# Kernel tuning notes

Measured on AMD Instinct MI355X. Metric: run time of the kernel, lower is better.

Reference implementation:

```python
import jax, jax.numpy as jnp
import numpy as np

B, S, SK = 4, 1024, 1024
Q_IN, KV_IN = 1024, 1024
G, DQ, DV = 16, 64, 64
OUT = Q_IN
EPS = 1e-5


def setup_inputs() -> dict:
    key = jax.random.key(0)
    ks = jax.random.split(key, 12)
    s_q = 1.0 / np.sqrt(Q_IN)
    s_kv = 1.0 / np.sqrt(KV_IN)
    s_p = 1.0 / np.sqrt(G * DV)
    return {
        "Q": jax.random.normal(ks[0], (B, S, Q_IN), jnp.float32),
        "KV": jax.random.normal(ks[1], (B, SK, KV_IN), jnp.float32),
        "Wq": jax.random.normal(ks[2], (G * DQ, Q_IN), jnp.float32) * s_q,
        "bq": jax.random.normal(ks[3], (G * DQ,), jnp.float32) * s_q,
        "Wk": jax.random.normal(ks[4], (G * DQ, KV_IN), jnp.float32) * s_kv,
        "bk": jax.random.normal(ks[5], (G * DQ,), jnp.float32) * s_kv,
        "Wv": jax.random.normal(ks[6], (G * DV, KV_IN), jnp.float32) * s_kv,
        "bv": jax.random.normal(ks[7], (G * DV,), jnp.float32) * s_kv,
        "Wp": jax.random.normal(ks[8], (OUT, G * DV), jnp.float32) * s_p,
        "bp": jax.random.normal(ks[9], (OUT,), jnp.float32) * s_p,
        "gamma": jnp.ones((OUT,), jnp.float32),
        "beta": jnp.zeros((OUT,), jnp.float32),
    }


def reference(Q, KV, Wq, bq, Wk, bk, Wv, bv, Wp, bp, gamma, beta):
    b, s, _ = Q.shape
    sk = KV.shape[1]
    inv_sqrt_dim = DQ ** (-0.5)

    # projections
    q = Q @ Wq.T + bq            # [b, s, G*DQ]
    k = KV @ Wk.T + bk           # [b, sk, G*DQ]
    v = KV @ Wv.T + bv           # [b, sk, G*DV]

    # q/k: group is the SLOW axis; v: group is the FAST axis (faithful to source)
    q = q.reshape(b, s, G, DQ)               # [b, s, g, d]
    k = k.reshape(b, sk, G, DQ)              # [b, sk, g, d]
    v = v.reshape(b, sk, DV, G)              # [b, sk, d, g]

    logits = jnp.einsum('bsgd,btgd->bgst', q, k) * inv_sqrt_dim  # [b, g, s, sk]
    scores = jax.nn.softmax(logits, axis=-1)
    attn = jnp.einsum('bgst,btdg->bgsd', scores, v)              # [b, g, s, dv]

    # flatten as (dv, g): feature index = d*G + g  (faithful to source permute)
    attn = attn.transpose(0, 2, 3, 1).reshape(b, s, DV * G)
    out = attn @ Wp.T + bp + Q

    # LayerNorm
    mu = out.mean(axis=-1, keepdims=True)
    var = out.var(axis=-1, keepdims=True)
    out = (out - mu) * jax.lax.rsqrt(var + EPS) * gamma + beta

    return out, scores.reshape(b * G, s, sk)
```

## Files before the change

### kernel.cpp

```cpp
#include <hip/hip_runtime.h>

typedef __attribute__((ext_vector_type(8))) short short8;
typedef __attribute__((ext_vector_type(4))) short s16x4;
typedef __attribute__((ext_vector_type(4))) float f32x4;
typedef __attribute__((ext_vector_type(2))) unsigned u32x2;

static __device__ __forceinline__ short f2bf(float x) {
  union { float f; unsigned u; } v; v.f = x;
  unsigned r = (v.u + 0x7fffu + ((v.u >> 16) & 1u)) >> 16;
  return (short)r;
}
static __device__ __forceinline__ unsigned cvtpk(float lo, float hi) {
  unsigned r;
  asm("v_cvt_pk_bf16_f32 %0, %1, %2" : "=v"(r) : "v"(lo), "v"(hi));
  return r;
}

static __device__ __forceinline__ void gld16(const short* g, short* l) {
  __builtin_amdgcn_global_load_lds(
      (const __attribute__((address_space(1))) unsigned*)g,
      (__attribute__((address_space(3))) unsigned*)l, 16, 0, 0);
}

static __device__ __forceinline__ void conv8(const float* __restrict__ src,
                                             short* __restrict__ dst, int i,
                                             float scale) {
  const f32x4* s = (const f32x4*)(src + (long)i * 8);
  f32x4 a = s[0], b = s[1];
  short8 o;
  o[0] = f2bf(a[0] * scale); o[1] = f2bf(a[1] * scale);
  o[2] = f2bf(a[2] * scale); o[3] = f2bf(a[3] * scale);
  o[4] = f2bf(b[0] * scale); o[5] = f2bf(b[1] * scale);
  o[6] = f2bf(b[2] * scale); o[7] = f2bf(b[3] * scale);
  *(short8*)(dst + (long)i * 8) = o;
}

__global__ __launch_bounds__(256) void prep(
    const float* __restrict__ Q, const float* __restrict__ KV,
    const float* __restrict__ Wq, const float* __restrict__ Wk,
    const float* __restrict__ Wv, const float* __restrict__ Wp,
    const float* __restrict__ bq,
    short* __restrict__ Qb, short* __restrict__ KVb,
    short* __restrict__ Wqb, short* __restrict__ Wkb,
    short* __restrict__ Wvb, short* __restrict__ Wpb,
    float* __restrict__ bqs) {
  const int blk = blockIdx.x, tid = threadIdx.x;
  if (blk < 2048) {
    conv8(Q, Qb, blk * 256 + tid, 1.f);
  } else if (blk < 4096) {
    conv8(KV, KVb, (blk - 2048) * 256 + tid, 1.f);
  } else if (blk < 4608) {
    conv8(Wq, Wqb, (blk - 4096) * 256 + tid, 0.125f);
  } else if (blk < 5120) {
    conv8(Wk, Wkb, (blk - 4608) * 256 + tid, 1.f);
  } else if (blk < 5632) {
    conv8(Wv, Wvb, (blk - 5120) * 256 + tid, 1.f);
  } else if (blk < 6656) {
    __shared__ float row[1024];
    const long o = blk - 5632;
    *(f32x4*)&row[tid * 4] = *(const f32x4*)(Wp + o * 1024 + tid * 4);
    __syncthreads();
    const int f0 = tid * 4;
    s16x4 t;
#pragma unroll
    for (int j = 0; j < 4; ++j) {
      int f = f0 + j;
      t[j] = f2bf(row[((f & 63) << 4) + (f >> 6)]);
    }
    *(s16x4*)(Wpb + o * 1024 + f0) = t;
  } else {
    int i = (blk - 6656) * 256 + tid;
    bqs[i] = bq[i] * 0.125f;
  }
}

template <typename OutT>
static __device__ __forceinline__ void gemm_core(
    const short* __restrict__ A, const short* __restrict__ B,
    OutT* __restrict__ C, const float* __restrict__ bias,
    const float* __restrict__ resid, int bm, int bn, int omode,
    short* Sm) {
  const int tid = threadIdx.x, lane = tid & 63, wave = tid >> 6;
  const int fr = lane & 15, khi = lane >> 4;
  const int wr = wave >> 1, wc = wave & 1;

  f32x4 acc[4][4];
#pragma unroll
  for (int m = 0; m < 4; ++m)
#pragma unroll
    for (int n = 0; n < 4; ++n) acc[m][n] = (f32x4){0.f, 0.f, 0.f, 0.f};

  auto stage = [&](int buf, int k0) {
    short* Asb = Sm + buf * 16384;
    short* Bsb = Asb + 8192;
#pragma unroll
    for (int it = 0; it < 4; ++it) {
      int l = it * 256 + tid;
      int r = l >> 3, c = (l & 7) ^ (r & 7);
      gld16(A + (long)(bm + r) * 1024 + k0 + c * 8, &Asb[l * 8]);
      gld16(B + (long)(bn + r) * 1024 + k0 + c * 8, &Bsb[l * 8]);
    }
  };

  stage(0, 0);
  __syncthreads();
  int cur = 0;
  for (int k0 = 0; k0 < 1024; k0 += 64) {
    if (k0 < 960) stage(cur ^ 1, k0 + 64);
    const short* Asb = Sm + cur * 16384;
    const short* Bsb = Asb + 8192;
#pragma unroll
    for (int ks = 0; ks < 64; ks += 32) {
      const int cc = (ks >> 3) + khi;
      short8 af[4], bf[4];
#pragma unroll
      for (int m = 0; m < 4; ++m) {
        const int ar = wr * 64 + m * 16 + fr;
        af[m] = *(const short8*)&Asb[ar * 64 + ((cc ^ (ar & 7)) * 8)];
      }
#pragma unroll
      for (int n = 0; n < 4; ++n) {
        const int br = wc * 64 + n * 16 + fr;
        bf[n] = *(const short8*)&Bsb[br * 64 + ((cc ^ (br & 7)) * 8)];
      }
#pragma unroll
      for (int m = 0; m < 4; ++m)
#pragma unroll
        for (int n = 0; n < 4; ++n)
          acc[m][n] = __builtin_amdgcn_mfma_f32_16x16x32_bf16(af[m], bf[n],
                                                              acc[m][n], 0, 0, 0);
    }
    __syncthreads();
    cur ^= 1;
  }

  const int col0 = fr, row0 = khi * 4;
  if constexpr (sizeof(OutT) == 2) {
#pragma unroll
    for (int m = 0; m < 4; ++m) {
#pragma unroll
      for (int n = 0; n < 4; ++n) {
        const int dgl = wc * 64 + n * 16 + col0;
        const float bi = bias[bn + dgl];
#pragma unroll
        for (int i = 0; i < 4; ++i) {
          const int tl = wr * 64 + m * 16 + row0 + i;
          const int a = (omode == 1) ? (dgl * 136 + tl) : (tl * 136 + dgl);
          Sm[a] = f2bf(acc[m][n][i] + bi);
        }
      }
    }
    __syncthreads();
    short* Cs = (short*)C;
#pragma unroll
    for (int it = 0; it < 8; ++it) {
      const int ch = it * 256 + tid;
      const int r = ch >> 4, cchunk = ch & 15;
      short8 v8 = *(const short8*)&Sm[r * 136 + cchunk * 8];
      long addr;
      if (omode == 0)
        addr = (long)(bm + r) * 1024 + bn + cchunk * 8;
      else
        addr = ((long)(bm >> 10) << 20) + ((long)(bn + r) << 10) + (bm & 1023) +
               cchunk * 8;
      *(short8*)(Cs + addr) = v8;
    }
  } else {
#pragma unroll
    for (int m = 0; m < 4; ++m) {
#pragma unroll
      for (int n = 0; n < 4; ++n) {
        const int gcol = bn + wc * 64 + n * 16 + col0;
        const float bi = bias[gcol];
#pragma unroll
        for (int i = 0; i < 4; ++i) {
          const int grow = bm + wr * 64 + m * 16 + row0 + i;
          float v = acc[m][n][i] + bi;
          if (resid) v += resid[(long)grow * 1024 + gcol];
          C[(long)grow * 1024 + gcol] = v;
        }
      }
    }
  }
}

__global__ __launch_bounds__(256, 2) void proj_all(
    const short* __restrict__ Qb, const short* __restrict__ KVb,
    const short* __restrict__ Wqb, const short* __restrict__ Wkb,
    const short* __restrict__ Wvb,
    const float* __restrict__ bqs, const float* __restrict__ bk,
    const float* __restrict__ bv,
    short* __restrict__ qb, short* __restrict__ kb, short* __restrict__ vt) {
  __shared__ short Sm[32768];
  int bid = blockIdx.x;
  int swz = (bid & 7) * 96 + (bid >> 3);
  const int seg = swz >> 8, local = swz & 255;
  const int bm = (local >> 3) * 128, bn = (local & 7) * 128;
  if (seg == 0)
    gemm_core<short>(Qb, Wqb, qb, bqs, nullptr, bm, bn, 0, Sm);
  else if (seg == 1)
    gemm_core<short>(KVb, Wkb, kb, bk, nullptr, bm, bn, 0, Sm);
  else
    gemm_core<short>(KVb, Wvb, vt, bv, nullptr, bm, bn, 1, Sm);
}

__global__ __launch_bounds__(256, 2) void out_gemm(
    const short* __restrict__ at, const short* __restrict__ Wpb,
    const float* __restrict__ bp, const float* __restrict__ Q,
    float* __restrict__ pre) {
  __shared__ short Sm[32768];
  int bid = blockIdx.x;
  int swz = (bid & 7) * 32 + (bid >> 3);
  const int bm = (swz >> 3) * 128, bn = (swz & 7) * 128;
  gemm_core<float>(at, Wpb, pre, bp, Q, bm, bn, 0, Sm);
}

__global__ __launch_bounds__(256, 3) void fused_attn(
    const short* __restrict__ qb,
    const short* __restrict__ kb,
    const short* __restrict__ vt,
    float* __restrict__ scores,
    short* __restrict__ at) {
  constexpr int LP = 72;
  __shared__ short Ks[2][64 * 64];
  __shared__ short Vs[2][64 * 64];
  __shared__ short Ps[128 * LP];

  int bid = blockIdx.x;
  bid = (bid & 7) * 64 + (bid >> 3);
  const int z = bid >> 3, b = z >> 4, g = z & 15;
  const int q0 = (bid & 7) * 128;

  const int tid = threadIdx.x, lane = tid & 63, w = tid >> 6;
  const int fr = lane & 15, khi = lane >> 4;
  const long bqk = (long)b << 20;
  const int qr = q0 + w * 32;

  short8 aq[4];
#pragma unroll
  for (int sub = 0; sub < 2; ++sub) {
    const short* qrow = qb + bqk + (long)(qr + sub * 16 + fr) * 1024 + g * 64 + khi * 8;
    aq[sub * 2] = *(const short8*)qrow;
    aq[sub * 2 + 1] = *(const short8*)(qrow + 32);
  }
  const short* kgp = kb + bqk + g * 64;
  const short* vgp = vt + bqk;

  auto stageK = [&](int buf, int t0) {
#pragma unroll
    for (int it = 0; it < 2; ++it) {
      int l = it * 256 + tid;
      int r = l >> 3, c = (l & 7) ^ ((l >> 5) & 7);
      gld16(kgp + (long)(t0 + r) * 1024 + c * 8, &Ks[buf][l * 8]);
    }
  };
  auto stageV = [&](int buf, int t0) {
#pragma unroll
    for (int it = 0; it < 2; ++it) {
      int l = it * 256 + tid;
      int r = l >> 3, c = (l & 7) ^ (r & 7);
      gld16(vgp + ((long)(r * 16 + g) << 10) + t0 + c * 8, &Vs[buf][l * 8]);
    }
  };

  const int xk = fr & 7;

  float s4[2][4] = {{0.f, 0.f, 0.f, 0.f}, {0.f, 0.f, 0.f, 0.f}};
  stageK(0, 0);
  __syncthreads();
  int cur = 0;
  for (int t0 = 0; t0 < 1024; t0 += 64) {
    if (t0 < 960) stageK(cur ^ 1, t0 + 64);
    f32x4 sacc[2][4];
#pragma unroll
    for (int sub = 0; sub < 2; ++sub)
#pragma unroll
      for (int nf = 0; nf < 4; ++nf) sacc[sub][nf] = (f32x4){0.f, 0.f, 0.f, 0.f};
#pragma unroll
    for (int nf = 0; nf < 4; ++nf) {
      const int r2 = fr * 4 + nf;
      short8 b0 = *(const short8*)&Ks[cur][r2 * 64 + ((khi ^ xk) * 8)];
      short8 b1 = *(const short8*)&Ks[cur][r2 * 64 + (((khi + 4) ^ xk) * 8)];
#pragma unroll
      for (int sub = 0; sub < 2; ++sub) {
        sacc[sub][nf] =
            __builtin_amdgcn_mfma_f32_16x16x32_bf16(aq[sub * 2], b0, sacc[sub][nf], 0, 0, 0);
        sacc[sub][nf] =
            __builtin_amdgcn_mfma_f32_16x16x32_bf16(aq[sub * 2 + 1], b1, sacc[sub][nf], 0, 0, 0);
      }
    }
#pragma unroll
    for (int sub = 0; sub < 2; ++sub)
#pragma unroll
      for (int nf = 0; nf < 4; ++nf)
#pragma unroll
        for (int i = 0; i < 4; ++i) s4[sub][i] += __expf(sacc[sub][nf][i]);
    __syncthreads();
    cur ^= 1;
  }
  float inv4[2][4];
#pragma unroll
  for (int sub = 0; sub < 2; ++sub)
#pragma unroll
    for (int i = 0; i < 4; ++i) {
      float s = s4[sub][i];
      s += __shfl_xor(s, 1);
      s += __shfl_xor(s, 2);
      s += __shfl_xor(s, 4);
      s += __shfl_xor(s, 8);
      inv4[sub][i] = 1.f / s;
    }

  f32x4 pacc[2][4];
#pragma unroll
  for (int sub = 0; sub < 2; ++sub)
#pragma unroll
    for (int nv = 0; nv < 4; ++nv) pacc[sub][nv] = (f32x4){0.f, 0.f, 0.f, 0.f};

  stageK(0, 0);
  stageV(0, 0);
  __syncthreads();
  cur = 0;
  for (int t0 = 0; t0 < 1024; t0 += 64) {
    if (t0 < 960) {
      stageK(cur ^ 1, t0 + 64);
      stageV(cur ^ 1, t0 + 64);
    }
    f32x4 sacc[2][4];
#pragma unroll
    for (int sub = 0; sub < 2; ++sub)
#pragma unroll
      for (int nf = 0; nf < 4; ++nf) sacc[sub][nf] = (f32x4){0.f, 0.f, 0.f, 0.f};
#pragma unroll
    for (int nf = 0; nf < 4; ++nf) {
      const int r2 = fr * 4 + nf;
      short8 b0 = *(const short8*)&Ks[cur][r2 * 64 + ((khi ^ xk) * 8)];
      short8 b1 = *(const short8*)&Ks[cur][r2 * 64 + (((khi + 4) ^ xk) * 8)];
#pragma unroll
      for (int sub = 0; sub < 2; ++sub) {
        sacc[sub][nf] =
            __builtin_amdgcn_mfma_f32_16x16x32_bf16(aq[sub * 2], b0, sacc[sub][nf], 0, 0, 0);
        sacc[sub][nf] =
            __builtin_amdgcn_mfma_f32_16x16x32_bf16(aq[sub * 2 + 1], b1, sacc[sub][nf], 0, 0, 0);
      }
    }
#pragma unroll
    for (int sub = 0; sub < 2; ++sub) {
#pragma unroll
      for (int i = 0; i < 4; ++i) {
        f32x4 o;
#pragma unroll
        for (int nf = 0; nf < 4; ++nf)
          o[nf] = __expf(sacc[sub][nf][i]) * inv4[sub][i];
        const int row = sub * 16 + khi * 4 + i;
        __builtin_nontemporal_store(
            o, (f32x4*)&scores[((long)z << 20) + ((long)(qr + row) << 10) + t0 + fr * 4]);
        u32x2 pp;
        pp[0] = cvtpk(o[0], o[1]);
        pp[1] = cvtpk(o[2], o[3]);
        *(u32x2*)&Ps[(w * 32 + row) * LP + fr * 4] = pp;
      }
    }

#pragma unroll
    for (int ks = 0; ks < 64; ks += 32) {
      const int cc = (ks >> 3) + khi;
      short8 ap[2];
#pragma unroll
      for (int sub = 0; sub < 2; ++sub)
        ap[sub] = *(const short8*)&Ps[(w * 32 + sub * 16 + fr) * LP + ks + khi * 8];
#pragma unroll
      for (int nv = 0; nv < 4; ++nv) {
        const int dr = nv * 16 + fr;
        short8 bvv = *(const short8*)&Vs[cur][dr * 64 + ((cc ^ (dr & 7)) * 8)];
#pragma unroll
        for (int sub = 0; sub < 2; ++sub)
          pacc[sub][nv] =
              __builtin_amdgcn_mfma_f32_16x16x32_bf16(ap[sub], bvv, pacc[sub][nv], 0, 0, 0);
      }
    }
    __syncthreads();
    cur ^= 1;
  }

#pragma unroll
  for (int sub = 0; sub < 2; ++sub)
#pragma unroll
    for (int nv = 0; nv < 4; ++nv)
#pragma unroll
      for (int i = 0; i < 4; ++i)
        Ps[(w * 32 + sub * 16 + khi * 4 + i) * LP + nv * 16 + fr] =
            f2bf(pacc[sub][nv][i]);
  const long atbase = bqk + ((long)qr << 10) + g * 64;
#pragma unroll
  for (int it = 0; it < 4; ++it) {
    const int ch = it * 64 + lane;
    const int row = ch >> 3, fc = ch & 7;
    s16x4 lo = *(const s16x4*)&Ps[(w * 32 + row) * LP + fc * 8];
    s16x4 hi = *(const s16x4*)&Ps[(w * 32 + row) * LP + fc * 8 + 4];
    short8 v8;
    v8[0] = lo[0]; v8[1] = lo[1]; v8[2] = lo[2]; v8[3] = lo[3];
    v8[4] = hi[0]; v8[5] = hi[1]; v8[6] = hi[2]; v8[7] = hi[3];
    *(short8*)(at + atbase + ((long)row << 10) + fc * 8) = v8;
  }
}

__global__ __launch_bounds__(256) void layernorm_rows(const float* __restrict__ X,
                                                      const float* __restrict__ gamma,
                                                      const float* __restrict__ beta,
                                                      float* __restrict__ O) {
  const int row = blockIdx.x * 4 + (threadIdx.x >> 6);
  const int lane = threadIdx.x & 63;
  const float* x = X + (long)row * 1024 + lane * 4;
  f32x4 v[4];
  float s = 0.f, sq = 0.f;
#pragma unroll
  for (int j = 0; j < 4; ++j) {
    v[j] = *(const f32x4*)(x + j * 256);
#pragma unroll
    for (int e = 0; e < 4; ++e) {
      s += v[j][e];
      sq += v[j][e] * v[j][e];
    }
  }
#pragma unroll
  for (int off = 32; off; off >>= 1) {
    s += __shfl_xor(s, off);
    sq += __shfl_xor(sq, off);
  }
  const float mu = s * (1.f / 1024.f);
  const float var = sq * (1.f / 1024.f) - mu * mu;
  const float rstd = rsqrtf(var + 1e-5f);
  float* o = O + (long)row * 1024 + lane * 4;
#pragma unroll
  for (int j = 0; j < 4; ++j) {
    f32x4 g = *(const f32x4*)(gamma + lane * 4 + j * 256);
    f32x4 be = *(const f32x4*)(beta + lane * 4 + j * 256);
    f32x4 r;
#pragma unroll
    for (int e = 0; e < 4; ++e) r[e] = (v[j][e] - mu) * rstd * g[e] + be[e];
    *(f32x4*)(o + j * 256) = r;
  }
}

extern "C" void kernel_launch(void* const* d_in, const int* in_sizes, int n_in,
                              void* d_out, int out_size, void* d_ws, size_t ws_size,
                              hipStream_t stream) {
  const float* Q = (const float*)d_in[0];
  const float* KV = (const float*)d_in[1];
  const float* Wq = (const float*)d_in[2];
  const float* bq = (const float*)d_in[3];
  const float* Wk = (const float*)d_in[4];
  const float* bk = (const float*)d_in[5];
  const float* Wv = (const float*)d_in[6];
  const float* bv = (const float*)d_in[7];
  const float* Wp = (const float*)d_in[8];
  const float* bp = (const float*)d_in[9];
  const float* gamma = (const float*)d_in[10];
  const float* beta = (const float*)d_in[11];

  float* out = (float*)d_out;
  float* scores = out + (long)4 * 1024 * 1024;

  char* ws = (char*)d_ws;
  short* Wqb = (short*)(ws);
  short* Wkb = (short*)(ws + (2L << 20));
  short* Wvb = (short*)(ws + (4L << 20));
  short* Wpb = (short*)(ws + (6L << 20));
  short* qb  = (short*)(ws + (8L << 20));
  short* kb  = (short*)(ws + (16L << 20));
  short* vt  = (short*)(ws + (24L << 20));
  short* at  = (short*)(ws + (32L << 20));
  float* pre = (float*)(ws + (40L << 20));
  short* Qb  = (short*)(ws + (40L << 20));
  short* KVb = (short*)(ws + (48L << 20));
  float* bqs = (float*)(ws + (56L << 20));
  (void)ws_size; (void)in_sizes; (void)n_in; (void)out_size;

  prep<<<6660, 256, 0, stream>>>(Q, KV, Wq, Wk, Wv, Wp, bq,
                                 Qb, KVb, Wqb, Wkb, Wvb, Wpb, bqs);

  proj_all<<<768, 256, 0, stream>>>(Qb, KVb, Wqb, Wkb, Wvb, bqs, bk, bv,
                                    qb, kb, vt);

  fused_attn<<<512, 256, 0, stream>>>(qb, kb, vt, scores, at);

  out_gemm<<<256, 256, 0, stream>>>(at, Wpb, bp, Q, pre);

  layernorm_rows<<<1024, 256, 0, stream>>>(pre, gamma, beta, out);
}
```

Baseline: 164.9 us.

## Split softmax row-sum pass into a separate higher-occupancy kernel

Moves the first attention pass, which computes the exp row sums of QK^T, out of the fused attention kernel into its own kernel. The new kernel uses 64-row query tiles, 1024 blocks and launch bounds of 4, and writes the inverse sums to a workspace buffer. The emit kernel then reads those inverses and runs only the second pass, which writes the scores and computes P·V. This is meant to give more parallelism and occupancy for the sum pass, at the cost of an extra launch, a small global round trip, and recomputing QK per 64-row tile with less reuse of K.

```diff
diff --git a/kernel.cpp b/kernel.cpp
--- a/kernel.cpp
+++ b/kernel.cpp
@@ -215,10 +215,76 @@
   gemm_core<float>(at, Wpb, pre, bp, Q, bm, bn, 0, Sm);
 }
 
-__global__ __launch_bounds__(256, 3) void fused_attn(
+__global__ __launch_bounds__(256, 4) void attn_sums(
+    const short* __restrict__ qb, const short* __restrict__ kb,
+    float* __restrict__ sinv) {
+  __shared__ short Ks[2][64 * 64];
+  int bid = blockIdx.x;
+  bid = (bid & 7) * 128 + (bid >> 3);
+  const int z = bid >> 4, b = z >> 4, g = z & 15;
+  const int q0 = (bid & 15) * 64;
+
+  const int tid = threadIdx.x, lane = tid & 63, w = tid >> 6;
+  const int fr = lane & 15, khi = lane >> 4;
+  const long bqk = (long)b << 20;
+  const int qr = q0 + w * 16;
+
+  const short* qrow = qb + bqk + (long)(qr + fr) * 1024 + g * 64 + khi * 8;
+  const short8 aq0 = *(const short8*)qrow;
+  const short8 aq1 = *(const short8*)(qrow + 32);
+  const short* kgp = kb + bqk + g * 64;
+
+  auto stageK = [&](int buf, int t0) {
+#pragma unroll
+    for (int it = 0; it < 2; ++it) {
+      int l = it * 256 + tid;
+      int r = l >> 3, c = (l & 7) ^ (r & 7);
+      gld16(kgp + (long)(t0 + r) * 1024 + c * 8, &Ks[buf][l * 8]);
+    }
+  };
+
+  float s4[4] = {0.f, 0.f, 0.f, 0.f};
+  stageK(0, 0);
+  __syncthreads();
+  int cur = 0;
+  const int xk = fr & 7;
+  for (int t0 = 0; t0 < 1024; t0 += 64) {
+    if (t0 < 960) stageK(cur ^ 1, t0 + 64);
+#pragma unroll
+    for (int nf = 0; nf < 4; ++nf) {
+      const int r2 = nf * 16 + fr;
+      short8 b0 = *(const short8*)&Ks[cur][r2 * 64 + ((khi ^ xk) * 8)];
+      short8 b1 = *(const short8*)&Ks[cur][r2 * 64 + (((khi + 4) ^ xk) * 8)];
+      f32x4 sacc = (f32x4){0.f, 0.f, 0.f, 0.f};
+      sacc = __builtin_amdgcn_mfma_f32_16x16x32_bf16(aq0, b0, sacc, 0, 0, 0);
+      sacc = __builtin_amdgcn_mfma_f32_16x16x32_bf16(aq1, b1, sacc, 0, 0, 0);
+#pragma unroll
+      for (int i = 0; i < 4; ++i) s4[i] += __expf(sacc[i]);
+    }
+    __syncthreads();
+    cur ^= 1;
+  }
+#pragma unroll
+  for (int i = 0; i < 4; ++i) {
+    float s = s4[i];
+    s += __shfl_xor(s, 1);
+    s += __shfl_xor(s, 2);
+    s += __shfl_xor(s, 4);
+    s += __shfl_xor(s, 8);
+    s4[i] = s;
+  }
+  if (fr == 0) {
+#pragma unroll
+    for (int i = 0; i < 4; ++i)
+      sinv[(long)z * 1024 + qr + khi * 4 + i] = 1.f / s4[i];
+  }
+}
+
+__global__ __launch_bounds__(256, 3) void attn_emit(
     const short* __restrict__ qb,
     const short* __restrict__ kb,
     const short* __restrict__ vt,
+    const float* __restrict__ sinv,
     float* __restrict__ scores,
     short* __restrict__ at) {
   constexpr int LP = 72;
@@ -243,6 +309,13 @@
     aq[sub * 2] = *(const short8*)qrow;
     aq[sub * 2 + 1] = *(const short8*)(qrow + 32);
   }
+  float inv4[2][4];
+#pragma unroll
+  for (int sub = 0; sub < 2; ++sub)
+#pragma unroll
+    for (int i = 0; i < 4; ++i)
+      inv4[sub][i] = sinv[(long)z * 1024 + qr + sub * 16 + khi * 4 + i];
+
   const short* kgp = kb + bqk + g * 64;
   const short* vgp = vt + bqk;
 
@@ -265,52 +338,6 @@
 
   const int xk = fr & 7;
 
-  float s4[2][4] = {{0.f, 0.f, 0.f, 0.f}, {0.f, 0.f, 0.f, 0.f}};
-  stageK(0, 0);
-  __syncthreads();
-  int cur = 0;
-  for (int t0 = 0; t0 < 1024; t0 += 64) {
-    if (t0 < 960) stageK(cur ^ 1, t0 + 64);
-    f32x4 sacc[2][4];
-#pragma unroll
-    for (int sub = 0; sub < 2; ++sub)
-#pragma unroll
-      for (int nf = 0; nf < 4; ++nf) sacc[sub][nf] = (f32x4){0.f, 0.f, 0.f, 0.f};
-#pragma unroll
-    for (int nf = 0; nf < 4; ++nf) {
-      const int r2 = fr * 4 + nf;
-      short8 b0 = *(const short8*)&Ks[cur][r2 * 64 + ((khi ^ xk) * 8)];
-      short8 b1 = *(const short8*)&Ks[cur][r2 * 64 + (((khi + 4) ^ xk) * 8)];
-#pragma unroll
-      for (int sub = 0; sub < 2; ++sub) {
-        sacc[sub][nf] =
-            __builtin_amdgcn_mfma_f32_16x16x32_bf16(aq[sub * 2], b0, sacc[sub][nf], 0, 0, 0);
-        sacc[sub][nf] =
-            __builtin_amdgcn_mfma_f32_16x16x32_bf16(aq[sub * 2 + 1], b1, sacc[sub][nf], 0, 0, 0);
-      }
-    }
-#pragma unroll
-    for (int sub = 0; sub < 2; ++sub)
-#pragma unroll
-      for (int nf = 0; nf < 4; ++nf)
-#pragma unroll
-        for (int i = 0; i < 4; ++i) s4[sub][i] += __expf(sacc[sub][nf][i]);
-    __syncthreads();
-    cur ^= 1;
-  }
-  float inv4[2][4];
-#pragma unroll
-  for (int sub = 0; sub < 2; ++sub)
-#pragma unroll
-    for (int i = 0; i < 4; ++i) {
-      float s = s4[sub][i];
-      s += __shfl_xor(s, 1);
-      s += __shfl_xor(s, 2);
-      s += __shfl_xor(s, 4);
-      s += __shfl_xor(s, 8);
-      inv4[sub][i] = 1.f / s;
-    }
-
   f32x4 pacc[2][4];
 #pragma unroll
   for (int sub = 0; sub < 2; ++sub)
@@ -320,7 +347,7 @@
   stageK(0, 0);
   stageV(0, 0);
   __syncthreads();
-  cur = 0;
+  int cur = 0;
   for (int t0 = 0; t0 < 1024; t0 += 64) {
     if (t0 < 960) {
       stageK(cur ^ 1, t0 + 64);
@@ -475,6 +502,7 @@
   short* Qb  = (short*)(ws + (40L << 20));
   short* KVb = (short*)(ws + (48L << 20));
   float* bqs = (float*)(ws + (56L << 20));
+  float* sinv = (float*)(ws + (56L << 20) + 65536);
   (void)ws_size; (void)in_sizes; (void)n_in; (void)out_size;
 
   prep<<<6660, 256, 0, stream>>>(Q, KV, Wq, Wk, Wv, Wp, bq,
@@ -483,7 +511,9 @@
   proj_all<<<768, 256, 0, stream>>>(Qb, KVb, Wqb, Wkb, Wvb, bqs, bk, bv,
                                     qb, kb, vt);
 
-  fused_attn<<<512, 256, 0, stream>>>(qb, kb, vt, scores, at);
+  attn_sums<<<1024, 256, 0, stream>>>(qb, kb, sinv);
+
+  attn_emit<<<512, 256, 0, stream>>>(qb, kb, vt, sinv, scores, at);
 
   out_gemm<<<256, 256, 0, stream>>>(at, Wpb, bp, Q, pre);
 
```

After: 167.1 us. About the same (+1.4%).

## Fuse fp32-to-bf16 activation conversion into projection GEMM and single-buffer attention

Applied to the files above, without the earlier changes.

The separate prep pass that converted Q and KV to bf16 is removed. The projection GEMM now loads fp32 activations directly, converts them in registers and writes bf16 into LDS, which saves a full write-and-reread of the activations through global memory. The catch is that A-tile staging becomes synchronous register loads instead of async global-to-LDS loads. Separately, fused_attn drops its K/V double buffering in favour of single buffers with a barrier per tile, and raises its occupancy hint from 3 to 4 blocks. This trades load/compute overlap for more resident waves.

```diff
diff --git a/kernel.cpp b/kernel.cpp
--- a/kernel.cpp
+++ b/kernel.cpp
@@ -36,28 +36,22 @@
 }
 
 __global__ __launch_bounds__(256) void prep(
-    const float* __restrict__ Q, const float* __restrict__ KV,
     const float* __restrict__ Wq, const float* __restrict__ Wk,
     const float* __restrict__ Wv, const float* __restrict__ Wp,
     const float* __restrict__ bq,
-    short* __restrict__ Qb, short* __restrict__ KVb,
     short* __restrict__ Wqb, short* __restrict__ Wkb,
     short* __restrict__ Wvb, short* __restrict__ Wpb,
     float* __restrict__ bqs) {
   const int blk = blockIdx.x, tid = threadIdx.x;
-  if (blk < 2048) {
-    conv8(Q, Qb, blk * 256 + tid, 1.f);
-  } else if (blk < 4096) {
-    conv8(KV, KVb, (blk - 2048) * 256 + tid, 1.f);
-  } else if (blk < 4608) {
-    conv8(Wq, Wqb, (blk - 4096) * 256 + tid, 0.125f);
-  } else if (blk < 5120) {
-    conv8(Wk, Wkb, (blk - 4608) * 256 + tid, 1.f);
-  } else if (blk < 5632) {
-    conv8(Wv, Wvb, (blk - 5120) * 256 + tid, 1.f);
-  } else if (blk < 6656) {
+  if (blk < 512) {
+    conv8(Wq, Wqb, blk * 256 + tid, 0.125f);
+  } else if (blk < 1024) {
+    conv8(Wk, Wkb, (blk - 512) * 256 + tid, 1.f);
+  } else if (blk < 1536) {
+    conv8(Wv, Wvb, (blk - 1024) * 256 + tid, 1.f);
+  } else if (blk < 2560) {
     __shared__ float row[1024];
-    const long o = blk - 5632;
+    const long o = blk - 1536;
     *(f32x4*)&row[tid * 4] = *(const f32x4*)(Wp + o * 1024 + tid * 4);
     __syncthreads();
     const int f0 = tid * 4;
@@ -69,14 +63,14 @@
     }
     *(s16x4*)(Wpb + o * 1024 + f0) = t;
   } else {
-    int i = (blk - 6656) * 256 + tid;
+    int i = (blk - 2560) * 256 + tid;
     bqs[i] = bq[i] * 0.125f;
   }
 }
 
-template <typename OutT>
+template <bool AF32, typename OutT>
 static __device__ __forceinline__ void gemm_core(
-    const short* __restrict__ A, const short* __restrict__ B,
+    const void* __restrict__ Ap, const short* __restrict__ B,
     OutT* __restrict__ C, const float* __restrict__ bias,
     const float* __restrict__ resid, int bm, int bn, int omode,
     short* Sm) {
@@ -84,6 +78,9 @@
   const int fr = lane & 15, khi = lane >> 4;
   const int wr = wave >> 1, wc = wave & 1;
 
+  const short* A16 = AF32 ? nullptr : (const short*)Ap;
+  const float* A32 = AF32 ? (const float*)Ap : nullptr;
+
   f32x4 acc[4][4];
 #pragma unroll
   for (int m = 0; m < 4; ++m)
@@ -97,7 +94,17 @@
     for (int it = 0; it < 4; ++it) {
       int l = it * 256 + tid;
       int r = l >> 3, c = (l & 7) ^ (r & 7);
-      gld16(A + (long)(bm + r) * 1024 + k0 + c * 8, &Asb[l * 8]);
+      if (!AF32) {
+        gld16(A16 + (long)(bm + r) * 1024 + k0 + c * 8, &Asb[l * 8]);
+      } else {
+        const float* p = A32 + (long)(bm + r) * 1024 + k0 + c * 8;
+        f32x4 x = *(const f32x4*)p, y = *(const f32x4*)(p + 4);
+        u32x2 lo, hi;
+        lo[0] = cvtpk(x[0], x[1]); lo[1] = cvtpk(x[2], x[3]);
+        hi[0] = cvtpk(y[0], y[1]); hi[1] = cvtpk(y[2], y[3]);
+        *(u32x2*)&Asb[l * 8] = lo;
+        *(u32x2*)&Asb[l * 8 + 4] = hi;
+      }
       gld16(B + (long)(bn + r) * 1024 + k0 + c * 8, &Bsb[l * 8]);
     }
   };
@@ -185,7 +192,7 @@
 }
 
 __global__ __launch_bounds__(256, 2) void proj_all(
-    const short* __restrict__ Qb, const short* __restrict__ KVb,
+    const float* __restrict__ Q, const float* __restrict__ KV,
     const short* __restrict__ Wqb, const short* __restrict__ Wkb,
     const short* __restrict__ Wvb,
     const float* __restrict__ bqs, const float* __restrict__ bk,
@@ -197,11 +204,11 @@
   const int seg = swz >> 8, local = swz & 255;
   const int bm = (local >> 3) * 128, bn = (local & 7) * 128;
   if (seg == 0)
-    gemm_core<short>(Qb, Wqb, qb, bqs, nullptr, bm, bn, 0, Sm);
+    gemm_core<true, short>(Q, Wqb, qb, bqs, nullptr, bm, bn, 0, Sm);
   else if (seg == 1)
-    gemm_core<short>(KVb, Wkb, kb, bk, nullptr, bm, bn, 0, Sm);
+    gemm_core<true, short>(KV, Wkb, kb, bk, nullptr, bm, bn, 0, Sm);
   else
-    gemm_core<short>(KVb, Wvb, vt, bv, nullptr, bm, bn, 1, Sm);
+    gemm_core<true, short>(KV, Wvb, vt, bv, nullptr, bm, bn, 1, Sm);
 }
 
 __global__ __launch_bounds__(256, 2) void out_gemm(
@@ -212,18 +219,18 @@
   int bid = blockIdx.x;
   int swz = (bid & 7) * 32 + (bid >> 3);
   const int bm = (swz >> 3) * 128, bn = (swz & 7) * 128;
-  gemm_core<float>(at, Wpb, pre, bp, Q, bm, bn, 0, Sm);
-}
-
-__global__ __launch_bounds__(256, 3) void fused_attn(
+  gemm_core<false, float>(at, Wpb, pre, bp, Q, bm, bn, 0, Sm);
+}
+
+__global__ __launch_bounds__(256, 4) void fused_attn(
     const short* __restrict__ qb,
     const short* __restrict__ kb,
     const short* __restrict__ vt,
     float* __restrict__ scores,
     short* __restrict__ at) {
   constexpr int LP = 72;
-  __shared__ short Ks[2][64 * 64];
-  __shared__ short Vs[2][64 * 64];
+  __shared__ short Ks[64 * 64];
+  __shared__ short Vs[64 * 64];
   __shared__ short Ps[128 * LP];
 
   int bid = blockIdx.x;
@@ -246,31 +253,29 @@
   const short* kgp = kb + bqk + g * 64;
   const short* vgp = vt + bqk;
 
-  auto stageK = [&](int buf, int t0) {
+  auto stageK = [&](int t0) {
 #pragma unroll
     for (int it = 0; it < 2; ++it) {
       int l = it * 256 + tid;
       int r = l >> 3, c = (l & 7) ^ ((l >> 5) & 7);
-      gld16(kgp + (long)(t0 + r) * 1024 + c * 8, &Ks[buf][l * 8]);
+      gld16(kgp + (long)(t0 + r) * 1024 + c * 8, &Ks[l * 8]);
     }
   };
-  auto stageV = [&](int buf, int t0) {
+  auto stageV = [&](int t0) {
 #pragma unroll
     for (int it = 0; it < 2; ++it) {
       int l = it * 256 + tid;
       int r = l >> 3, c = (l & 7) ^ (r & 7);
-      gld16(vgp + ((long)(r * 16 + g) << 10) + t0 + c * 8, &Vs[buf][l * 8]);
+      gld16(vgp + ((long)(r * 16 + g) << 10) + t0 + c * 8, &Vs[l * 8]);
     }
   };
 
   const int xk = fr & 7;
 
   float s4[2][4] = {{0.f, 0.f, 0.f, 0.f}, {0.f, 0.f, 0.f, 0.f}};
-  stageK(0, 0);
-  __syncthreads();
-  int cur = 0;
   for (int t0 = 0; t0 < 1024; t0 += 64) {
-    if (t0 < 960) stageK(cur ^ 1, t0 + 64);
+    stageK(t0);
+    __syncthreads();
     f32x4 sacc[2][4];
 #pragma unroll
     for (int sub = 0; sub < 2; ++sub)
@@ -279,8 +284,8 @@
 #pragma unroll
     for (int nf = 0; nf < 4; ++nf) {
       const int r2 = fr * 4 + nf;
-      short8 b0 = *(const short8*)&Ks[cur][r2 * 64 + ((khi ^ xk) * 8)];
-      short8 b1 = *(const short8*)&Ks[cur][r2 * 64 + (((khi + 4) ^ xk) * 8)];
+      short8 b0 = *(const short8*)&Ks[r2 * 64 + ((khi ^ xk) * 8)];
+      short8 b1 = *(const short8*)&Ks[r2 * 64 + (((khi + 4) ^ xk) * 8)];
 #pragma unroll
       for (int sub = 0; sub < 2; ++sub) {
         sacc[sub][nf] =
@@ -296,7 +301,6 @@
 #pragma unroll
         for (int i = 0; i < 4; ++i) s4[sub][i] += __expf(sacc[sub][nf][i]);
     __syncthreads();
-    cur ^= 1;
   }
   float inv4[2][4];
 #pragma unroll
@@ -317,15 +321,10 @@
 #pragma unroll
     for (int nv = 0; nv < 4; ++nv) pacc[sub][nv] = (f32x4){0.f, 0.f, 0.f, 0.f};
 
-  stageK(0, 0);
-  stageV(0, 0);
-  __syncthreads();
-  cur = 0;
   for (int t0 = 0; t0 < 1024; t0 += 64) {
-    if (t0 < 960) {
-      stageK(cur ^ 1, t0 + 64);
-      stageV(cur ^ 1, t0 + 64);
-    }
+    stageK(t0);
+    stageV(t0);
+    __syncthreads();
     f32x4 sacc[2][4];
 #pragma unroll
     for (int sub = 0; sub < 2; ++sub)
@@ -334,8 +333,8 @@
 #pragma unroll
     for (int nf = 0; nf < 4; ++nf) {
       const int r2 = fr * 4 + nf;
-      short8 b0 = *(const short8*)&Ks[cur][r2 * 64 + ((khi ^ xk) * 8)];
-      short8 b1 = *(const short8*)&Ks[cur][r2 * 64 + (((khi + 4) ^ xk) * 8)];
+      short8 b0 = *(const short8*)&Ks[r2 * 64 + ((khi ^ xk) * 8)];
+      short8 b1 = *(const short8*)&Ks[r2 * 64 + (((khi + 4) ^ xk) * 8)];
 #pragma unroll
       for (int sub = 0; sub < 2; ++sub) {
         sacc[sub][nf] =
@@ -372,7 +371,7 @@
 #pragma unroll
       for (int nv = 0; nv < 4; ++nv) {
         const int dr = nv * 16 + fr;
-        short8 bvv = *(const short8*)&Vs[cur][dr * 64 + ((cc ^ (dr & 7)) * 8)];
+        short8 bvv = *(const short8*)&Vs[dr * 64 + ((cc ^ (dr & 7)) * 8)];
 #pragma unroll
         for (int sub = 0; sub < 2; ++sub)
           pacc[sub][nv] =
@@ -380,7 +379,6 @@
       }
     }
     __syncthreads();
-    cur ^= 1;
   }
 
 #pragma unroll
@@ -472,15 +470,12 @@
   short* vt  = (short*)(ws + (24L << 20));
   short* at  = (short*)(ws + (32L << 20));
   float* pre = (float*)(ws + (40L << 20));
-  short* Qb  = (short*)(ws + (40L << 20));
-  short* KVb = (short*)(ws + (48L << 20));
   float* bqs = (float*)(ws + (56L << 20));
   (void)ws_size; (void)in_sizes; (void)n_in; (void)out_size;
 
-  prep<<<6660, 256, 0, stream>>>(Q, KV, Wq, Wk, Wv, Wp, bq,
-                                 Qb, KVb, Wqb, Wkb, Wvb, Wpb, bqs);
-
-  proj_all<<<768, 256, 0, stream>>>(Qb, KVb, Wqb, Wkb, Wvb, bqs, bk, bv,
+  prep<<<2564, 256, 0, stream>>>(Wq, Wk, Wv, Wp, bq, Wqb, Wkb, Wvb, Wpb, bqs);
+
+  proj_all<<<768, 256, 0, stream>>>(Q, KV, Wqb, Wkb, Wvb, bqs, bk, bv,
                                     qb, kb, vt);
 
   fused_attn<<<512, 256, 0, stream>>>(qb, kb, vt, scores, at);
```

Result: slower. 186.5 us (+13.1%).

## Use 8 waves of 16 query rows each in fused attention

Applied to the files above, without the earlier changes.

The fused attention kernel now runs 512 threads per block, and each of the 8 waves handles 16 query rows instead of 32. Each thread issues one K/V staging load per tile instead of two. Per-wave register use drops, which allows more resident waves to hide the exp and scores-store latency. The cost is that each wave reuses each K/V LDS fragment for half as many MFMAs, and block-wide barriers now synchronise more waves.

```diff
diff --git a/kernel.cpp b/kernel.cpp
--- a/kernel.cpp
+++ b/kernel.cpp
@@ -215,7 +215,7 @@
   gemm_core<float>(at, Wpb, pre, bp, Q, bm, bn, 0, Sm);
 }
 
-__global__ __launch_bounds__(256, 3) void fused_attn(
+__global__ __launch_bounds__(512, 4) void fused_attn(
     const short* __restrict__ qb,
     const short* __restrict__ kb,
     const short* __restrict__ vt,
@@ -234,88 +234,63 @@
   const int tid = threadIdx.x, lane = tid & 63, w = tid >> 6;
   const int fr = lane & 15, khi = lane >> 4;
   const long bqk = (long)b << 20;
-  const int qr = q0 + w * 32;
-
-  short8 aq[4];
-#pragma unroll
-  for (int sub = 0; sub < 2; ++sub) {
-    const short* qrow = qb + bqk + (long)(qr + sub * 16 + fr) * 1024 + g * 64 + khi * 8;
-    aq[sub * 2] = *(const short8*)qrow;
-    aq[sub * 2 + 1] = *(const short8*)(qrow + 32);
-  }
+  const int qr = q0 + w * 16;
+
+  const short* qrow = qb + bqk + (long)(qr + fr) * 1024 + g * 64 + khi * 8;
+  const short8 aq0 = *(const short8*)qrow;
+  const short8 aq1 = *(const short8*)(qrow + 32);
   const short* kgp = kb + bqk + g * 64;
   const short* vgp = vt + bqk;
 
   auto stageK = [&](int buf, int t0) {
-#pragma unroll
-    for (int it = 0; it < 2; ++it) {
-      int l = it * 256 + tid;
-      int r = l >> 3, c = (l & 7) ^ ((l >> 5) & 7);
-      gld16(kgp + (long)(t0 + r) * 1024 + c * 8, &Ks[buf][l * 8]);
-    }
+    int r = tid >> 3, c = (tid & 7) ^ ((tid >> 5) & 7);
+    gld16(kgp + (long)(t0 + r) * 1024 + c * 8, &Ks[buf][tid * 8]);
   };
   auto stageV = [&](int buf, int t0) {
-#pragma unroll
-    for (int it = 0; it < 2; ++it) {
-      int l = it * 256 + tid;
-      int r = l >> 3, c = (l & 7) ^ (r & 7);
-      gld16(vgp + ((long)(r * 16 + g) << 10) + t0 + c * 8, &Vs[buf][l * 8]);
-    }
+    int r = tid >> 3, c = (tid & 7) ^ (r & 7);
+    gld16(vgp + ((long)(r * 16 + g) << 10) + t0 + c * 8, &Vs[buf][tid * 8]);
   };
 
   const int xk = fr & 7;
 
-  float s4[2][4] = {{0.f, 0.f, 0.f, 0.f}, {0.f, 0.f, 0.f, 0.f}};
+  float s4[4] = {0.f, 0.f, 0.f, 0.f};
   stageK(0, 0);
   __syncthreads();
   int cur = 0;
   for (int t0 = 0; t0 < 1024; t0 += 64) {
     if (t0 < 960) stageK(cur ^ 1, t0 + 64);
-    f32x4 sacc[2][4];
-#pragma unroll
-    for (int sub = 0; sub < 2; ++sub)
-#pragma unroll
-      for (int nf = 0; nf < 4; ++nf) sacc[sub][nf] = (f32x4){0.f, 0.f, 0.f, 0.f};
+    f32x4 sacc[4];
+#pragma unroll
+    for (int nf = 0; nf < 4; ++nf) sacc[nf] = (f32x4){0.f, 0.f, 0.f, 0.f};
 #pragma unroll
     for (int nf = 0; nf < 4; ++nf) {
       const int r2 = fr * 4 + nf;
       short8 b0 = *(const short8*)&Ks[cur][r2 * 64 + ((khi ^ xk) * 8)];
       short8 b1 = *(const short8*)&Ks[cur][r2 * 64 + (((khi + 4) ^ xk) * 8)];
-#pragma unroll
-      for (int sub = 0; sub < 2; ++sub) {
-        sacc[sub][nf] =
-            __builtin_amdgcn_mfma_f32_16x16x32_bf16(aq[sub * 2], b0, sacc[sub][nf], 0, 0, 0);
-        sacc[sub][nf] =
-            __builtin_amdgcn_mfma_f32_16x16x32_bf16(aq[sub * 2 + 1], b1, sacc[sub][nf], 0, 0, 0);
-      }
-    }
-#pragma unroll
-    for (int sub = 0; sub < 2; ++sub)
-#pragma unroll
-      for (int nf = 0; nf < 4; ++nf)
-#pragma unroll
-        for (int i = 0; i < 4; ++i) s4[sub][i] += __expf(sacc[sub][nf][i]);
+      sacc[nf] = __builtin_amdgcn_mfma_f32_16x16x32_bf16(aq0, b0, sacc[nf], 0, 0, 0);
+      sacc[nf] = __builtin_amdgcn_mfma_f32_16x16x32_bf16(aq1, b1, sacc[nf], 0, 0, 0);
+    }
+#pragma unroll
+    for (int nf = 0; nf < 4; ++nf)
+#pragma unroll
+      for (int i = 0; i < 4; ++i) s4[i] += __expf(sacc[nf][i]);
     __syncthreads();
     cur ^= 1;
   }
-  float inv4[2][4];
-#pragma unroll
-  for (int sub = 0; sub < 2; ++sub)
-#pragma unroll
-    for (int i = 0; i < 4; ++i) {
-      float s = s4[sub][i];
-      s += __shfl_xor(s, 1);
-      s += __shfl_xor(s, 2);
-      s += __shfl_xor(s, 4);
-      s += __shfl_xor(s, 8);
-      inv4[sub][i] = 1.f / s;
-    }
-
-  f32x4 pacc[2][4];
-#pragma unroll
-  for (int sub = 0; sub < 2; ++sub)
-#pragma unroll
-    for (int nv = 0; nv < 4; ++nv) pacc[sub][nv] = (f32x4){0.f, 0.f, 0.f, 0.f};
+  float inv4[4];
+#pragma unroll
+  for (int i = 0; i < 4; ++i) {
+    float s = s4[i];
+    s += __shfl_xor(s, 1);
+    s += __shfl_xor(s, 2);
+    s += __shfl_xor(s, 4);
+    s += __shfl_xor(s, 8);
+    inv4[i] = 1.f / s;
+  }
+
+  f32x4 pacc[4];
+#pragma unroll
+  for (int nv = 0; nv < 4; ++nv) pacc[nv] = (f32x4){0.f, 0.f, 0.f, 0.f};
 
   stageK(0, 0);
   stageV(0, 0);
@@ -326,57 +301,41 @@
       stageK(cur ^ 1, t0 + 64);
       stageV(cur ^ 1, t0 + 64);
     }
-    f32x4 sacc[2][4];
-#pragma unroll
-    for (int sub = 0; sub < 2; ++sub)
-#pragma unroll
-      for (int nf = 0; nf < 4; ++nf) sacc[sub][nf] = (f32x4){0.f, 0.f, 0.f, 0.f};
+    f32x4 sacc[4];
+#pragma unroll
+    for (int nf = 0; nf < 4; ++nf) sacc[nf] = (f32x4){0.f, 0.f, 0.f, 0.f};
 #pragma unroll
     for (int nf = 0; nf < 4; ++nf) {
       const int r2 = fr * 4 + nf;
       short8 b0 = *(const short8*)&Ks[cur][r2 * 64 + ((khi ^ xk) * 8)];
       short8 b1 = *(const short8*)&Ks[cur][r2 * 64 + (((khi + 4) ^ xk) * 8)];
-#pragma unroll
-      for (int sub = 0; sub < 2; ++sub) {
-        sacc[sub][nf] =
-            __builtin_amdgcn_mfma_f32_16x16x32_bf16(aq[sub * 2], b0, sacc[sub][nf], 0, 0, 0);
-        sacc[sub][nf] =
-            __builtin_amdgcn_mfma_f32_16x16x32_bf16(aq[sub * 2 + 1], b1, sacc[sub][nf], 0, 0, 0);
-      }
-    }
-#pragma unroll
-    for (int sub = 0; sub < 2; ++sub) {
-#pragma unroll
-      for (int i = 0; i < 4; ++i) {
-        f32x4 o;
-#pragma unroll
-        for (int nf = 0; nf < 4; ++nf)
-          o[nf] = __expf(sacc[sub][nf][i]) * inv4[sub][i];
-        const int row = sub * 16 + khi * 4 + i;
-        __builtin_nontemporal_store(
-            o, (f32x4*)&scores[((long)z << 20) + ((long)(qr + row) << 10) + t0 + fr * 4]);
-        u32x2 pp;
-        pp[0] = cvtpk(o[0], o[1]);
-        pp[1] = cvtpk(o[2], o[3]);
-        *(u32x2*)&Ps[(w * 32 + row) * LP + fr * 4] = pp;
-      }
+      sacc[nf] = __builtin_amdgcn_mfma_f32_16x16x32_bf16(aq0, b0, sacc[nf], 0, 0, 0);
+      sacc[nf] = __builtin_amdgcn_mfma_f32_16x16x32_bf16(aq1, b1, sacc[nf], 0, 0, 0);
+    }
+#pragma unroll
+    for (int i = 0; i < 4; ++i) {
+      f32x4 o;
+#pragma unroll
+      for (int nf = 0; nf < 4; ++nf)
+        o[nf] = __expf(sacc[nf][i]) * inv4[i];
+      const int row = khi * 4 + i;
+      __builtin_nontemporal_store(
+          o, (f32x4*)&scores[((long)z << 20) + ((long)(qr + row) << 10) + t0 + fr * 4]);
+      u32x2 pp;
+      pp[0] = cvtpk(o[0], o[1]);
+      pp[1] = cvtpk(o[2], o[3]);
+      *(u32x2*)&Ps[(w * 16 + row) * LP + fr * 4] = pp;
     }
 
 #pragma unroll
     for (int ks = 0; ks < 64; ks += 32) {
       const int cc = (ks >> 3) + khi;
-      short8 ap[2];
-#pragma unroll
-      for (int sub = 0; sub < 2; ++sub)
-        ap[sub] = *(const short8*)&Ps[(w * 32 + sub * 16 + fr) * LP + ks + khi * 8];
+      short8 ap = *(const short8*)&Ps[(w * 16 + fr) * LP + ks + khi * 8];
 #pragma unroll
       for (int nv = 0; nv < 4; ++nv) {
         const int dr = nv * 16 + fr;
         short8 bvv = *(const short8*)&Vs[cur][dr * 64 + ((cc ^ (dr & 7)) * 8)];
-#pragma unroll
-        for (int sub = 0; sub < 2; ++sub)
-          pacc[sub][nv] =
-              __builtin_amdgcn_mfma_f32_16x16x32_bf16(ap[sub], bvv, pacc[sub][nv], 0, 0, 0);
+        pacc[nv] = __builtin_amdgcn_mfma_f32_16x16x32_bf16(ap, bvv, pacc[nv], 0, 0, 0);
       }
     }
     __syncthreads();
@@ -384,20 +343,17 @@
   }
 
 #pragma unroll
-  for (int sub = 0; sub < 2; ++sub)
-#pragma unroll
-    for (int nv = 0; nv < 4; ++nv)
-#pragma unroll
-      for (int i = 0; i < 4; ++i)
-        Ps[(w * 32 + sub * 16 + khi * 4 + i) * LP + nv * 16 + fr] =
-            f2bf(pacc[sub][nv][i]);
+  for (int nv = 0; nv < 4; ++nv)
+#pragma unroll
+    for (int i = 0; i < 4; ++i)
+      Ps[(w * 16 + khi * 4 + i) * LP + nv * 16 + fr] = f2bf(pacc[nv][i]);
   const long atbase = bqk + ((long)qr << 10) + g * 64;
 #pragma unroll
-  for (int it = 0; it < 4; ++it) {
+  for (int it = 0; it < 2; ++it) {
     const int ch = it * 64 + lane;
     const int row = ch >> 3, fc = ch & 7;
-    s16x4 lo = *(const s16x4*)&Ps[(w * 32 + row) * LP + fc * 8];
-    s16x4 hi = *(const s16x4*)&Ps[(w * 32 + row) * LP + fc * 8 + 4];
+    s16x4 lo = *(const s16x4*)&Ps[(w * 16 + row) * LP + fc * 8];
+    s16x4 hi = *(const s16x4*)&Ps[(w * 16 + row) * LP + fc * 8 + 4];
     short8 v8;
     v8[0] = lo[0]; v8[1] = lo[1]; v8[2] = lo[2]; v8[3] = lo[3];
     v8[4] = hi[0]; v8[5] = hi[1]; v8[6] = hi[2]; v8[7] = hi[3];
@@ -483,7 +439,7 @@
   proj_all<<<768, 256, 0, stream>>>(Qb, KVb, Wqb, Wkb, Wvb, bqs, bk, bv,
                                     qb, kb, vt);
 
-  fused_attn<<<512, 256, 0, stream>>>(qb, kb, vt, scores, at);
+  fused_attn<<<512, 512, 0, stream>>>(qb, kb, vt, scores, at);
 
   out_gemm<<<256, 256, 0, stream>>>(at, Wpb, bp, Q, pre);
 
```

Result: no change. 162.2 us, median of 2 (-1.6%).
